# Optimization experiments

Measured on AMD Instinct MI355X. Metric: run time of the kernel, lower is better.

The kernel has to match this reference:

```python
import jax, jax.numpy as jnp
import numpy as np

D_MODEL = 1024
NUM_HEADS = 16
D_K = D_MODEL // NUM_HEADS


def setup_inputs() -> dict:
    key = jax.random.key(0)
    ks = jax.random.split(key, 12)
    B, S = 2, 2048
    s = 1.0 / np.sqrt(D_MODEL)
    inp = {
        "query": jax.random.normal(ks[0], (B, S, D_MODEL), jnp.float32),
        "key": jax.random.normal(ks[1], (B, S, D_MODEL), jnp.float32),
        "value": jax.random.normal(ks[2], (B, S, D_MODEL), jnp.float32),
        "Wq": jax.random.normal(ks[3], (D_MODEL, D_MODEL), jnp.float32) * s,
        "bq": jax.random.normal(ks[4], (D_MODEL,), jnp.float32) * s,
        "Wk": jax.random.normal(ks[5], (D_MODEL, D_MODEL), jnp.float32) * s,
        "bk": jax.random.normal(ks[6], (D_MODEL,), jnp.float32) * s,
        "Wv": jax.random.normal(ks[7], (D_MODEL, D_MODEL), jnp.float32) * s,
        "bv": jax.random.normal(ks[8], (D_MODEL,), jnp.float32) * s,
        "Wo": jax.random.normal(ks[9], (D_MODEL, D_MODEL), jnp.float32) * s,
        "bo": jax.random.normal(ks[10], (D_MODEL,), jnp.float32) * s,
    }
    return inp


def _split_heads(x):
    B, S, _ = x.shape
    return x.reshape(B, S, NUM_HEADS, D_K).transpose(0, 2, 1, 3)  # [B,H,S,Dk]


def reference(query, key, value, Wq, bq, Wk, bk, Wv, bv, Wo, bo):
    # Linear projections (torch Linear: x @ W.T + b)
    Q = _split_heads(query @ Wq.T + bq)
    K = _split_heads(key @ Wk.T + bk)
    V = _split_heads(value @ Wv.T + bv)
    scale = 1.0 / jnp.sqrt(jnp.asarray(D_K, Q.dtype))
    scores = jnp.einsum('bhqd,bhkd->bhqk', Q, K) * scale  # [B,H,S,S]
    attn = jax.nn.softmax(scores, axis=-1)
    # dropout is identity in eval mode
    x = jnp.einsum('bhqk,bhkd->bhqd', attn, V)
    B, H, S, Dk = x.shape
    x = x.transpose(0, 2, 1, 3).reshape(B, S, H * Dk)
    return x @ Wo.T + bo
```

## Files before the change

kernel.cpp:

```cpp
#include <hip/hip_runtime.h>
#include <hip/hip_bf16.h>

typedef __bf16 bf16;
typedef __attribute__((ext_vector_type(4))) __bf16 bf16x4;
typedef __attribute__((ext_vector_type(8))) __bf16 bf16x8;
typedef __attribute__((ext_vector_type(4))) float f32x4;
typedef __attribute__((ext_vector_type(16))) float f32x16;
typedef unsigned int u32;

#define D_MODEL 1024
#define NHEADS 16
#define DK 64
#define BATCH 2
#define SEQ 2048
#define NTOK (BATCH * SEQ)

#define QSCALE 0.18033688011112042f

__device__ __forceinline__ u32 cvtpk_bf16(float lo, float hi) {
  u32 r;
  asm("v_cvt_pk_bf16_f32 %0, %1, %2" : "=v"(r) : "v"(lo), "v"(hi));
  return r;
}
__device__ __forceinline__ void plswap(u32& a, u32& b) {
  asm("v_permlane32_swap_b32 %0, %1" : "+v"(a), "+v"(b));
}
__device__ __forceinline__ float fast_exp2(float x) {
#if __has_builtin(__builtin_amdgcn_exp2f)
  return __builtin_amdgcn_exp2f(x);
#else
  return exp2f(x);
#endif
}
__device__ __forceinline__ float xhalf_add(float x) {
  return x + __shfl_xor(x, 32);
}

__device__ __forceinline__ int frag_off_q(int s, int d) {
  return ((s >> 5) << 11) + ((d >> 4) << 9) + ((((d >> 3) & 1) * 32 + (s & 31)) << 3) + (d & 7);
}
__device__ __forceinline__ int frag_off_k(int s, int d) {
  return ((s >> 6) << 12) + ((((s >> 5) & 1) * 4 + (d >> 4)) << 9) +
         ((((d >> 3) & 1) * 32 + (s & 31)) << 3) + (d & 7);
}
__device__ __forceinline__ int frag_off_v(int s, int d) {
  return ((s >> 6) << 12) + (((d >> 5) * 4 + ((s >> 4) & 3)) << 9) +
         ((((s >> 3) & 1) * 32 + (d & 31)) << 3) + (s & 7);
}

__global__ __launch_bounds__(256) void cvt3_kernel(
    const float* __restrict__ s0, const float* __restrict__ s1, const float* __restrict__ s2,
    bf16* __restrict__ d0, bf16* __restrict__ d1, bf16* __restrict__ d2, int n4) {
  int i = blockIdx.x * blockDim.x + threadIdx.x;
  if (i >= n4) return;
  const float* s = blockIdx.y == 0 ? s0 : blockIdx.y == 1 ? s1 : s2;
  bf16* d = blockIdx.y == 0 ? d0 : blockIdx.y == 1 ? d1 : d2;
  float4 v = reinterpret_cast<const float4*>(s)[i];
  bf16x4 o;
  o[0] = (bf16)v.x; o[1] = (bf16)v.y; o[2] = (bf16)v.z; o[3] = (bf16)v.w;
  reinterpret_cast<bf16x4*>(d)[i] = o;
}

__global__ __launch_bounds__(256) void cvt4_kernel(
    const float* __restrict__ s0, const float* __restrict__ s1,
    const float* __restrict__ s2, const float* __restrict__ s3,
    bf16* __restrict__ d0, bf16* __restrict__ d1, bf16* __restrict__ d2, bf16* __restrict__ d3,
    int n4) {
  int i = blockIdx.x * blockDim.x + threadIdx.x;
  if (i >= n4) return;
  const float* s = blockIdx.y == 0 ? s0 : blockIdx.y == 1 ? s1 : blockIdx.y == 2 ? s2 : s3;
  bf16* d = blockIdx.y == 0 ? d0 : blockIdx.y == 1 ? d1 : blockIdx.y == 2 ? d2 : d3;
  float4 v = reinterpret_cast<const float4*>(s)[i];
  bf16x4 o;
  o[0] = (bf16)v.x; o[1] = (bf16)v.y; o[2] = (bf16)v.z; o[3] = (bf16)v.w;
  reinterpret_cast<bf16x4*>(d)[i] = o;
}

#define ASYNC_COPY16(gptr, lptr)                                                \
  __builtin_amdgcn_global_load_lds(                                             \
      (__attribute__((address_space(1))) void*)(gptr),                          \
      (__attribute__((address_space(3))) void*)(lptr), 16, 0, 0)

struct ProjArgs {
  const bf16* A[3];
  const bf16* W[3];
  const float* bias[3];
  bf16* out[3];
};

__global__ __launch_bounds__(256) void gemm_proj(ProjArgs pa, int K) {
  __shared__ bf16 As[128][32];
  __shared__ bf16 Bs[128][32];
  const int z = blockIdx.z;
  const bf16* A = pa.A[z];
  const bf16* Bw = pa.W[z];
  const int m0 = blockIdx.x * 128;
  const int n0 = blockIdx.y * 128;

  const int t = threadIdx.x;
  const int wave = t >> 6;
  const int lane = t & 63;
  const int wr = (wave >> 1) * 64;
  const int wc = (wave & 1) * 64;
  const int r4 = lane >> 2;
  const int c8 = (lane & 3) * 8;
  const int fr = lane & 15;
  const int fk = (lane >> 4) * 8;

  f32x4 acc[4][4] = {};

  for (int k0 = 0; k0 < K; k0 += 32) {
    ASYNC_COPY16(&A[(size_t)(m0 + wave * 16 + r4) * K + k0 + c8], &As[wave * 16][0]);
    ASYNC_COPY16(&A[(size_t)(m0 + 64 + wave * 16 + r4) * K + k0 + c8], &As[64 + wave * 16][0]);
    ASYNC_COPY16(&Bw[(size_t)(n0 + wave * 16 + r4) * K + k0 + c8], &Bs[wave * 16][0]);
    ASYNC_COPY16(&Bw[(size_t)(n0 + 64 + wave * 16 + r4) * K + k0 + c8], &Bs[64 + wave * 16][0]);
    __syncthreads();

    bf16x8 af[4], bfr[4];
#pragma unroll
    for (int m = 0; m < 4; m++)
      af[m] = *reinterpret_cast<const bf16x8*>(&As[wr + m * 16 + fr][fk]);
#pragma unroll
    for (int n = 0; n < 4; n++)
      bfr[n] = *reinterpret_cast<const bf16x8*>(&Bs[wc + n * 16 + fr][fk]);
#pragma unroll
    for (int m = 0; m < 4; m++)
#pragma unroll
      for (int n = 0; n < 4; n++)
        acc[m][n] = __builtin_amdgcn_mfma_f32_16x16x32_bf16(af[m], bfr[n], acc[m][n], 0, 0, 0);
    __syncthreads();
  }

  const float scale = (z == 0) ? QSCALE : 1.0f;
  const float* bias = pa.bias[z];
  bf16* out = pa.out[z];
#pragma unroll
  for (int m = 0; m < 4; m++) {
#pragma unroll
    for (int n = 0; n < 4; n++) {
      const int col = n0 + wc + n * 16 + fr;
      const float bv = bias[col];
#pragma unroll
      for (int j = 0; j < 4; j++) {
        const int row = m0 + wr + m * 16 + (lane >> 4) * 4 + j;
        const float v = (acc[m][n][j] + bv) * scale;
        const int b = row >> 11;
        const int s = row & (SEQ - 1);
        const int h = col >> 6;
        const int d = col & (DK - 1);
        const size_t base = (size_t)(b * NHEADS + h) * SEQ * DK;
        int off;
        if (z == 0)      off = frag_off_q(s, d);
        else if (z == 1) off = frag_off_k(s, d);
        else             off = frag_off_v(s, d);
        out[base + off] = (bf16)v;
      }
    }
  }
}

__global__ __launch_bounds__(256) void gemm_out(
    const bf16* __restrict__ A, const bf16* __restrict__ Bw,
    const float* __restrict__ bias, float* __restrict__ out, int K) {
  __shared__ bf16 As[128][32];
  __shared__ bf16 Bs[128][32];
  const int m0 = blockIdx.x * 128;
  const int n0 = blockIdx.y * 128;

  const int t = threadIdx.x;
  const int wave = t >> 6;
  const int lane = t & 63;
  const int wr = (wave >> 1) * 64;
  const int wc = (wave & 1) * 64;
  const int r4 = lane >> 2;
  const int c8 = (lane & 3) * 8;
  const int fr = lane & 15;
  const int fk = (lane >> 4) * 8;

  f32x4 acc[4][4] = {};

  for (int k0 = 0; k0 < K; k0 += 32) {
    ASYNC_COPY16(&A[(size_t)(m0 + wave * 16 + r4) * K + k0 + c8], &As[wave * 16][0]);
    ASYNC_COPY16(&A[(size_t)(m0 + 64 + wave * 16 + r4) * K + k0 + c8], &As[64 + wave * 16][0]);
    ASYNC_COPY16(&Bw[(size_t)(n0 + wave * 16 + r4) * K + k0 + c8], &Bs[wave * 16][0]);
    ASYNC_COPY16(&Bw[(size_t)(n0 + 64 + wave * 16 + r4) * K + k0 + c8], &Bs[64 + wave * 16][0]);
    __syncthreads();

    bf16x8 af[4], bfr[4];
#pragma unroll
    for (int m = 0; m < 4; m++)
      af[m] = *reinterpret_cast<const bf16x8*>(&As[wr + m * 16 + fr][fk]);
#pragma unroll
    for (int n = 0; n < 4; n++)
      bfr[n] = *reinterpret_cast<const bf16x8*>(&Bs[wc + n * 16 + fr][fk]);
#pragma unroll
    for (int m = 0; m < 4; m++)
#pragma unroll
      for (int n = 0; n < 4; n++)
        acc[m][n] = __builtin_amdgcn_mfma_f32_16x16x32_bf16(af[m], bfr[n], acc[m][n], 0, 0, 0);
    __syncthreads();
  }

#pragma unroll
  for (int m = 0; m < 4; m++) {
#pragma unroll
    for (int n = 0; n < 4; n++) {
      const int col = n0 + wc + n * 16 + fr;
      const float bv = bias[col];
#pragma unroll
      for (int j = 0; j < 4; j++) {
        const int row = m0 + wr + m * 16 + (lane >> 4) * 4 + j;
        out[(size_t)row * D_MODEL + col] = acc[m][n][j] + bv;
      }
    }
  }
}

#define QBLK 32
#define KVBLK 32
#define NT (SEQ / KVBLK)

__global__ __launch_bounds__(256, 2) void attn_kernel(
    const bf16* __restrict__ Qf,
    const bf16* __restrict__ Kf,
    const bf16* __restrict__ Vf,
    bf16* __restrict__ X) {
  const int lane = threadIdx.x & 63;
  const int wave = threadIdx.x >> 6;

  const int i = blockIdx.x;
  const int xcd = i & 7;
  const int slot = i >> 3;
  const int hgrp = slot >> 4;
  const int xq = slot & 15;
  const int bh = xcd + 8 * hgrp;
  const int bb = bh >> 4, hh = bh & (NHEADS - 1);
  const int q0 = xq * (QBLK * 4) + wave * QBLK;
  const int row = lane & 31, hi = lane >> 5;

  const bf16* Qp = Qf + (size_t)bh * SEQ * DK + (size_t)q0 * DK;
  const bf16* Kp = Kf + (size_t)bh * SEQ * DK;
  const bf16* Vp = Vf + (size_t)bh * SEQ * DK;

  bf16x8 qf[4];
#pragma unroll
  for (int kd = 0; kd < 4; kd++)
    qf[kd] = *reinterpret_cast<const bf16x8*>(&Qp[kd * 512 + lane * 8]);

  f32x16 ot0, ot1, fz;
#pragma unroll
  for (int r = 0; r < 16; r++) { ot0[r] = 0.f; ot1[r] = 0.f; fz[r] = 0.f; }
  float l_run = 0.f;

  bf16x8 ka[4], kb[4];

#define LOADK32(dst, tt)                                                        \
  {                                                                             \
    const bf16* kbase_ = Kp + (size_t)(tt) * 2048 + lane * 8;                   \
    _Pragma("unroll") for (int kd = 0; kd < 4; kd++)                            \
        dst[kd] = *reinterpret_cast<const bf16x8*>(&kbase_[kd * 512]);          \
  }

  LOADK32(ka, 0)
  LOADK32(kb, 1)
  f32x16 sa, sb;
  __builtin_amdgcn_s_setprio(1);
  sa = __builtin_amdgcn_mfma_f32_32x32x16_bf16(ka[0], qf[0], fz, 0, 0, 0);
#pragma unroll
  for (int kd = 1; kd < 4; kd++)
    sa = __builtin_amdgcn_mfma_f32_32x32x16_bf16(ka[kd], qf[kd], sa, 0, 0, 0);
  __builtin_amdgcn_s_setprio(0);

  auto pipe = [&](f32x16& SC, f32x16& SN, bf16x8 (&KN)[4], bf16x8 (&KL)[4], int tc) {
    __builtin_amdgcn_s_setprio(1);
    SN = __builtin_amdgcn_mfma_f32_32x32x16_bf16(KN[0], qf[0], fz, 0, 0, 0);
#pragma unroll
    for (int kd = 1; kd < 4; kd++)
      SN = __builtin_amdgcn_mfma_f32_32x32x16_bf16(KN[kd], qf[kd], SN, 0, 0, 0);
    __builtin_amdgcn_s_setprio(0);

    LOADK32(KL, (tc + 2) & (NT - 1))

    bf16x8 vf[2][2];
    {
      const bf16* vbase_ = Vp + (size_t)(tc >> 1) * 4096 + lane * 8;
      const int so = (tc & 1) * 2;
#pragma unroll
      for (int dh = 0; dh < 2; dh++)
#pragma unroll
        for (int ks = 0; ks < 2; ks++)
          vf[dh][ks] = *reinterpret_cast<const bf16x8*>(
              &vbase_[(dh * 4 + so + ks) * 512]);
    }

    float p[16];
#pragma unroll
    for (int r = 0; r < 16; r++) p[r] = fast_exp2(SC[r]);
    float a8[8];
#pragma unroll
    for (int r = 0; r < 8; r++) a8[r] = p[r] + p[r + 8];
#pragma unroll
    for (int r = 0; r < 4; r++) a8[r] += a8[r + 4];
    l_run += (a8[0] + a8[1]) + (a8[2] + a8[3]);

    u32 c[8];
#pragma unroll
    for (int i2 = 0; i2 < 8; i2++) c[i2] = cvtpk_bf16(p[2 * i2], p[2 * i2 + 1]);
    plswap(c[0], c[2]);   plswap(c[1], c[3]);
    plswap(c[4], c[6]);   plswap(c[5], c[7]);
    bf16x8 pbv[2];
#pragma unroll
    for (int ks = 0; ks < 2; ks++) {
      union { u32 u[4]; bf16x8 v; } pk;
      pk.u[0] = c[ks * 4 + 0]; pk.u[1] = c[ks * 4 + 1];
      pk.u[2] = c[ks * 4 + 2]; pk.u[3] = c[ks * 4 + 3];
      pbv[ks] = pk.v;
    }

    __builtin_amdgcn_s_setprio(1);
    ot0 = __builtin_amdgcn_mfma_f32_32x32x16_bf16(vf[0][0], pbv[0], ot0, 0, 0, 0);
    ot0 = __builtin_amdgcn_mfma_f32_32x32x16_bf16(vf[0][1], pbv[1], ot0, 0, 0, 0);
    ot1 = __builtin_amdgcn_mfma_f32_32x32x16_bf16(vf[1][0], pbv[0], ot1, 0, 0, 0);
    ot1 = __builtin_amdgcn_mfma_f32_32x32x16_bf16(vf[1][1], pbv[1], ot1, 0, 0, 0);
    __builtin_amdgcn_s_setprio(0);
  };

  for (int t = 0; t < NT; t += 2) {
    pipe(sa, sb, kb, ka, t);
    pipe(sb, sa, ka, kb, t + 1);
  }

  l_run = xhalf_add(l_run);

  const float inv = 1.0f / l_run;
  bf16* Xp = X + ((size_t)bb * SEQ + q0 + row) * D_MODEL + hh * DK;
#pragma unroll
  for (int g = 0; g < 4; g++) {
    bf16x4 w0, w1;
#pragma unroll
    for (int j = 0; j < 4; j++) {
      w0[j] = (bf16)(ot0[g * 4 + j] * inv);
      w1[j] = (bf16)(ot1[g * 4 + j] * inv);
    }
    *reinterpret_cast<bf16x4*>(&Xp[g * 8 + hi * 4]) = w0;
    *reinterpret_cast<bf16x4*>(&Xp[32 + g * 8 + hi * 4]) = w1;
  }
}

extern "C" void kernel_launch(void* const* d_in, const int* in_sizes, int n_in,
                              void* d_out, int out_size, void* d_ws, size_t ws_size,
                              hipStream_t stream) {
  const float* q  = (const float*)d_in[0];
  const float* k  = (const float*)d_in[1];
  const float* v  = (const float*)d_in[2];
  const float* Wq = (const float*)d_in[3];
  const float* bq = (const float*)d_in[4];
  const float* Wk = (const float*)d_in[5];
  const float* bk = (const float*)d_in[6];
  const float* Wv = (const float*)d_in[7];
  const float* bv = (const float*)d_in[8];
  const float* Wo = (const float*)d_in[9];
  const float* bo = (const float*)d_in[10];

  char* ws = (char*)d_ws;
  size_t off = 0;
  auto alloc = [&](size_t bytes) -> void* {
    void* p = ws + off;
    off += (bytes + 255) & ~(size_t)255;
    return p;
  };
  const size_t ACT = (size_t)NTOK * D_MODEL;
  const size_t WEL = (size_t)D_MODEL * D_MODEL;

  bf16* Xq  = (bf16*)alloc(ACT * 2);
  bf16* Xk  = (bf16*)alloc(ACT * 2);
  bf16* Xv  = (bf16*)alloc(ACT * 2);
  bf16* Wqb = (bf16*)alloc(WEL * 2);
  bf16* Wkb = (bf16*)alloc(WEL * 2);
  bf16* Wvb = (bf16*)alloc(WEL * 2);
  bf16* Wob = (bf16*)alloc(WEL * 2);
  bf16* Qfb = (bf16*)alloc(ACT * 2);
  bf16* Kfb = (bf16*)alloc(ACT * 2);
  bf16* Vfb = (bf16*)alloc(ACT * 2);
  bf16* Xa  = (bf16*)alloc(ACT * 2);

  {
    int n4 = (int)(ACT / 4);
    cvt3_kernel<<<dim3((n4 + 255) / 256, 3), dim3(256), 0, stream>>>(q, k, v, Xq, Xk, Xv, n4);
  }
  {
    int n4 = (int)(WEL / 4);
    cvt4_kernel<<<dim3((n4 + 255) / 256, 4), dim3(256), 0, stream>>>(
        Wq, Wk, Wv, Wo, Wqb, Wkb, Wvb, Wob, n4);
  }

  ProjArgs pa;
  pa.A[0] = Xq;  pa.A[1] = Xk;  pa.A[2] = Xv;
  pa.W[0] = Wqb; pa.W[1] = Wkb; pa.W[2] = Wvb;
  pa.bias[0] = bq; pa.bias[1] = bk; pa.bias[2] = bv;
  pa.out[0] = Qfb; pa.out[1] = Kfb; pa.out[2] = Vfb;
  gemm_proj<<<dim3(NTOK / 128, D_MODEL / 128, 3), dim3(256), 0, stream>>>(pa, D_MODEL);

  attn_kernel<<<dim3(512), dim3(256), 0, stream>>>(Qfb, Kfb, Vfb, Xa);

  gemm_out<<<dim3(NTOK / 128, D_MODEL / 128), dim3(256), 0, stream>>>(
      Xa, Wob, bo, (float*)d_out, D_MODEL);
}
```

Before: 134.0 us.

## Process two query tiles per wave to reuse K/V register loads

Each wave now handles two 32-row query tiles (q0 and q0+128) against the same K and V fragments, halving global K/V loads per query row. The grid shrinks from 512 to 256 blocks and launch bounds drop to one block per CU to make room for the extra accumulators. V loads are also prefetched one tile ahead into double buffers. The cost is fewer resident waves for hiding latency and only 256 blocks to fill the device.

New measurement: 132.9 us. No clear change (-0.8%).

```diff
diff --git a/kernel.cpp b/kernel.cpp
--- a/kernel.cpp
+++ b/kernel.cpp
@@ -220,7 +220,7 @@
 #define KVBLK 32
 #define NT (SEQ / KVBLK)
 
-__global__ __launch_bounds__(256, 2) void attn_kernel(
+__global__ __launch_bounds__(256, 1) void attn_kernel(
     const bf16* __restrict__ Qf,
     const bf16* __restrict__ Kf,
     const bf16* __restrict__ Vf,
@@ -231,28 +231,31 @@
   const int i = blockIdx.x;
   const int xcd = i & 7;
   const int slot = i >> 3;
-  const int hgrp = slot >> 4;
-  const int xq = slot & 15;
+  const int hgrp = slot >> 3;
+  const int qb = slot & 7;
   const int bh = xcd + 8 * hgrp;
   const int bb = bh >> 4, hh = bh & (NHEADS - 1);
-  const int q0 = xq * (QBLK * 4) + wave * QBLK;
+  const int q0 = qb * 256 + wave * QBLK;
+  const int q1 = q0 + 128;
   const int row = lane & 31, hi = lane >> 5;
 
-  const bf16* Qp = Qf + (size_t)bh * SEQ * DK + (size_t)q0 * DK;
+  const bf16* Qp = Qf + (size_t)bh * SEQ * DK;
   const bf16* Kp = Kf + (size_t)bh * SEQ * DK;
   const bf16* Vp = Vf + (size_t)bh * SEQ * DK;
 
-  bf16x8 qf[4];
-#pragma unroll
-  for (int kd = 0; kd < 4; kd++)
-    qf[kd] = *reinterpret_cast<const bf16x8*>(&Qp[kd * 512 + lane * 8]);
-
-  f32x16 ot0, ot1, fz;
-#pragma unroll
-  for (int r = 0; r < 16; r++) { ot0[r] = 0.f; ot1[r] = 0.f; fz[r] = 0.f; }
-  float l_run = 0.f;
-
-  bf16x8 ka[4], kb[4];
+  bf16x8 qfA[4], qfB[4];
+#pragma unroll
+  for (int kd = 0; kd < 4; kd++) {
+    qfA[kd] = *reinterpret_cast<const bf16x8*>(&Qp[(size_t)q0 * DK + kd * 512 + lane * 8]);
+    qfB[kd] = *reinterpret_cast<const bf16x8*>(&Qp[(size_t)q1 * DK + kd * 512 + lane * 8]);
+  }
+
+  f32x16 oA0, oA1, oB0, oB1, fz;
+#pragma unroll
+  for (int r = 0; r < 16; r++) { oA0[r] = 0.f; oA1[r] = 0.f; oB0[r] = 0.f; oB1[r] = 0.f; fz[r] = 0.f; }
+  float lA = 0.f, lB = 0.f;
+
+  bf16x8 ka[4], kb[4], va[4], vb[4];
 
 #define LOADK32(dst, tt)                                                        \
   {                                                                             \
@@ -260,90 +263,114 @@
     _Pragma("unroll") for (int kd = 0; kd < 4; kd++)                            \
         dst[kd] = *reinterpret_cast<const bf16x8*>(&kbase_[kd * 512]);          \
   }
+#define LOADV32(dst, tt)                                                        \
+  {                                                                             \
+    const bf16* vbase_ = Vp + (size_t)((tt) >> 1) * 4096 + ((tt) & 1) * 1024 +  \
+                         lane * 8;                                              \
+    dst[0] = *reinterpret_cast<const bf16x8*>(&vbase_[0]);                      \
+    dst[1] = *reinterpret_cast<const bf16x8*>(&vbase_[512]);                    \
+    dst[2] = *reinterpret_cast<const bf16x8*>(&vbase_[2048]);                   \
+    dst[3] = *reinterpret_cast<const bf16x8*>(&vbase_[2560]);                   \
+  }
 
   LOADK32(ka, 0)
   LOADK32(kb, 1)
-  f32x16 sa, sb;
-  __builtin_amdgcn_s_setprio(1);
-  sa = __builtin_amdgcn_mfma_f32_32x32x16_bf16(ka[0], qf[0], fz, 0, 0, 0);
-#pragma unroll
-  for (int kd = 1; kd < 4; kd++)
-    sa = __builtin_amdgcn_mfma_f32_32x32x16_bf16(ka[kd], qf[kd], sa, 0, 0, 0);
-  __builtin_amdgcn_s_setprio(0);
-
-  auto pipe = [&](f32x16& SC, f32x16& SN, bf16x8 (&KN)[4], bf16x8 (&KL)[4], int tc) {
+  LOADV32(va, 0)
+
+  auto body = [&](int tc, bf16x8 (&KC)[4], bf16x8 (&VC)[4], bf16x8 (&VN)[4]) {
+    f32x16 sA, sB;
     __builtin_amdgcn_s_setprio(1);
-    SN = __builtin_amdgcn_mfma_f32_32x32x16_bf16(KN[0], qf[0], fz, 0, 0, 0);
+    sA = __builtin_amdgcn_mfma_f32_32x32x16_bf16(KC[0], qfA[0], fz, 0, 0, 0);
 #pragma unroll
     for (int kd = 1; kd < 4; kd++)
-      SN = __builtin_amdgcn_mfma_f32_32x32x16_bf16(KN[kd], qf[kd], SN, 0, 0, 0);
+      sA = __builtin_amdgcn_mfma_f32_32x32x16_bf16(KC[kd], qfA[kd], sA, 0, 0, 0);
+    sB = __builtin_amdgcn_mfma_f32_32x32x16_bf16(KC[0], qfB[0], fz, 0, 0, 0);
+#pragma unroll
+    for (int kd = 1; kd < 4; kd++)
+      sB = __builtin_amdgcn_mfma_f32_32x32x16_bf16(KC[kd], qfB[kd], sB, 0, 0, 0);
     __builtin_amdgcn_s_setprio(0);
 
-    LOADK32(KL, (tc + 2) & (NT - 1))
-
-    bf16x8 vf[2][2];
+    LOADK32(KC, (tc + 2) & (NT - 1))
+    LOADV32(VN, (tc + 1) & (NT - 1))
+
     {
-      const bf16* vbase_ = Vp + (size_t)(tc >> 1) * 4096 + lane * 8;
-      const int so = (tc & 1) * 2;
-#pragma unroll
-      for (int dh = 0; dh < 2; dh++)
-#pragma unroll
-        for (int ks = 0; ks < 2; ks++)
-          vf[dh][ks] = *reinterpret_cast<const bf16x8*>(
-              &vbase_[(dh * 4 + so + ks) * 512]);
+      float p[16];
+#pragma unroll
+      for (int r = 0; r < 16; r++) p[r] = fast_exp2(sA[r]);
+      float a8[8];
+#pragma unroll
+      for (int r = 0; r < 8; r++) a8[r] = p[r] + p[r + 8];
+#pragma unroll
+      for (int r = 0; r < 4; r++) a8[r] += a8[r + 4];
+      lA += (a8[0] + a8[1]) + (a8[2] + a8[3]);
+      u32 c[8];
+#pragma unroll
+      for (int i2 = 0; i2 < 8; i2++) c[i2] = cvtpk_bf16(p[2 * i2], p[2 * i2 + 1]);
+      plswap(c[0], c[2]); plswap(c[1], c[3]);
+      plswap(c[4], c[6]); plswap(c[5], c[7]);
+      union { u32 u[4]; bf16x8 v; } pk0, pk1;
+      pk0.u[0] = c[0]; pk0.u[1] = c[1]; pk0.u[2] = c[2]; pk0.u[3] = c[3];
+      pk1.u[0] = c[4]; pk1.u[1] = c[5]; pk1.u[2] = c[6]; pk1.u[3] = c[7];
+      __builtin_amdgcn_s_setprio(1);
+      oA0 = __builtin_amdgcn_mfma_f32_32x32x16_bf16(VC[0], pk0.v, oA0, 0, 0, 0);
+      oA0 = __builtin_amdgcn_mfma_f32_32x32x16_bf16(VC[1], pk1.v, oA0, 0, 0, 0);
+      oA1 = __builtin_amdgcn_mfma_f32_32x32x16_bf16(VC[2], pk0.v, oA1, 0, 0, 0);
+      oA1 = __builtin_amdgcn_mfma_f32_32x32x16_bf16(VC[3], pk1.v, oA1, 0, 0, 0);
+      __builtin_amdgcn_s_setprio(0);
     }
-
-    float p[16];
-#pragma unroll
-    for (int r = 0; r < 16; r++) p[r] = fast_exp2(SC[r]);
-    float a8[8];
-#pragma unroll
-    for (int r = 0; r < 8; r++) a8[r] = p[r] + p[r + 8];
-#pragma unroll
-    for (int r = 0; r < 4; r++) a8[r] += a8[r + 4];
-    l_run += (a8[0] + a8[1]) + (a8[2] + a8[3]);
-
-    u32 c[8];
-#pragma unroll
-    for (int i2 = 0; i2 < 8; i2++) c[i2] = cvtpk_bf16(p[2 * i2], p[2 * i2 + 1]);
-    plswap(c[0], c[2]);   plswap(c[1], c[3]);
-    plswap(c[4], c[6]);   plswap(c[5], c[7]);
-    bf16x8 pbv[2];
-#pragma unroll
-    for (int ks = 0; ks < 2; ks++) {
-      union { u32 u[4]; bf16x8 v; } pk;
-      pk.u[0] = c[ks * 4 + 0]; pk.u[1] = c[ks * 4 + 1];
-      pk.u[2] = c[ks * 4 + 2]; pk.u[3] = c[ks * 4 + 3];
-      pbv[ks] = pk.v;
+    {
+      float p[16];
+#pragma unroll
+      for (int r = 0; r < 16; r++) p[r] = fast_exp2(sB[r]);
+      float a8[8];
+#pragma unroll
+      for (int r = 0; r < 8; r++) a8[r] = p[r] + p[r + 8];
+#pragma unroll
+      for (int r = 0; r < 4; r++) a8[r] += a8[r + 4];
+      lB += (a8[0] + a8[1]) + (a8[2] + a8[3]);
+      u32 c[8];
+#pragma unroll
+      for (int i2 = 0; i2 < 8; i2++) c[i2] = cvtpk_bf16(p[2 * i2], p[2 * i2 + 1]);
+      plswap(c[0], c[2]); plswap(c[1], c[3]);
+      plswap(c[4], c[6]); plswap(c[5], c[7]);
+      union { u32 u[4]; bf16x8 v; } pk0, pk1;
+      pk0.u[0] = c[0]; pk0.u[1] = c[1]; pk0.u[2] = c[2]; pk0.u[3] = c[3];
+      pk1.u[0] = c[4]; pk1.u[1] = c[5]; pk1.u[2] = c[6]; pk1.u[3] = c[7];
+      __builtin_amdgcn_s_setprio(1);
+      oB0 = __builtin_amdgcn_mfma_f32_32x32x16_bf16(VC[0], pk0.v, oB0, 0, 0, 0);
+      oB0 = __builtin_amdgcn_mfma_f32_32x32x16_bf16(VC[1], pk1.v, oB0, 0, 0, 0);
+      oB1 = __builtin_amdgcn_mfma_f32_32x32x16_bf16(VC[2], pk0.v, oB1, 0, 0, 0);
+      oB1 = __builtin_amdgcn_mfma_f32_32x32x16_bf16(VC[3], pk1.v, oB1, 0, 0, 0);
+      __builtin_amdgcn_s_setprio(0);
     }
-
-    __builtin_amdgcn_s_setprio(1);
-    ot0 = __builtin_amdgcn_mfma_f32_32x32x16_bf16(vf[0][0], pbv[0], ot0, 0, 0, 0);
-    ot0 = __builtin_amdgcn_mfma_f32_32x32x16_bf16(vf[0][1], pbv[1], ot0, 0, 0, 0);
-    ot1 = __builtin_amdgcn_mfma_f32_32x32x16_bf16(vf[1][0], pbv[0], ot1, 0, 0, 0);
-    ot1 = __builtin_amdgcn_mfma_f32_32x32x16_bf16(vf[1][1], pbv[1], ot1, 0, 0, 0);
-    __builtin_amdgcn_s_setprio(0);
   };
 
   for (int t = 0; t < NT; t += 2) {
-    pipe(sa, sb, kb, ka, t);
-    pipe(sb, sa, ka, kb, t + 1);
-  }
-
-  l_run = xhalf_add(l_run);
-
-  const float inv = 1.0f / l_run;
-  bf16* Xp = X + ((size_t)bb * SEQ + q0 + row) * D_MODEL + hh * DK;
+    body(t, ka, va, vb);
+    body(t + 1, kb, vb, va);
+  }
+
+  lA = xhalf_add(lA);
+  lB = xhalf_add(lB);
+
+  const float invA = 1.0f / lA;
+  const float invB = 1.0f / lB;
+  bf16* XpA = X + ((size_t)bb * SEQ + q0 + row) * D_MODEL + hh * DK;
+  bf16* XpB = X + ((size_t)bb * SEQ + q1 + row) * D_MODEL + hh * DK;
 #pragma unroll
   for (int g = 0; g < 4; g++) {
-    bf16x4 w0, w1;
+    bf16x4 w0, w1, w2, w3;
 #pragma unroll
     for (int j = 0; j < 4; j++) {
-      w0[j] = (bf16)(ot0[g * 4 + j] * inv);
-      w1[j] = (bf16)(ot1[g * 4 + j] * inv);
+      w0[j] = (bf16)(oA0[g * 4 + j] * invA);
+      w1[j] = (bf16)(oA1[g * 4 + j] * invA);
+      w2[j] = (bf16)(oB0[g * 4 + j] * invB);
+      w3[j] = (bf16)(oB1[g * 4 + j] * invB);
     }
-    *reinterpret_cast<bf16x4*>(&Xp[g * 8 + hi * 4]) = w0;
-    *reinterpret_cast<bf16x4*>(&Xp[32 + g * 8 + hi * 4]) = w1;
+    *reinterpret_cast<bf16x4*>(&XpA[g * 8 + hi * 4]) = w0;
+    *reinterpret_cast<bf16x4*>(&XpA[32 + g * 8 + hi * 4]) = w1;
+    *reinterpret_cast<bf16x4*>(&XpB[g * 8 + hi * 4]) = w2;
+    *reinterpret_cast<bf16x4*>(&XpB[32 + g * 8 + hi * 4]) = w3;
   }
 }
 
@@ -401,7 +428,7 @@
   pa.out[0] = Qfb; pa.out[1] = Kfb; pa.out[2] = Vfb;
   gemm_proj<<<dim3(NTOK / 128, D_MODEL / 128, 3), dim3(256), 0, stream>>>(pa, D_MODEL);
 
-  attn_kernel<<<dim3(512), dim3(256), 0, stream>>>(Qfb, Kfb, Vfb, Xa);
+  attn_kernel<<<dim3(256), dim3(256), 0, stream>>>(Qfb, Kfb, Vfb, Xa);
 
   gemm_out<<<dim3(NTOK / 128, D_MODEL / 128), dim3(256), 0, stream>>>(
       Xa, Wob, bo, (float*)d_out, D_MODEL);
```
